# Kernel tuning notes

Measured on AMD Instinct MI355X. Metric: run time of the kernel, lower is better.

The kernel has to match this reference:

```python
import jax, jax.numpy as jnp
import numpy as np

C = 1024
H = 16
DH = C // H
T = 2048
B = 2
EPS = 1e-5


def setup_inputs() -> dict:
    key = jax.random.key(0)
    ks = jax.random.split(key, 11)
    s = 1.0 / np.sqrt(C)
    return {
        "x": jax.random.normal(ks[0], (B, C, T), dtype=jnp.float32),
        "Wq": jax.random.normal(ks[1], (C, C), dtype=jnp.float32) * s,
        "bq": jax.random.normal(ks[2], (C,), dtype=jnp.float32) * 0.01,
        "Wk": jax.random.normal(ks[3], (C, C), dtype=jnp.float32) * s,
        "bk": jax.random.normal(ks[4], (C,), dtype=jnp.float32) * 0.01,
        "Wv": jax.random.normal(ks[5], (C, C), dtype=jnp.float32) * s,
        "bv": jax.random.normal(ks[6], (C,), dtype=jnp.float32) * 0.01,
        "Wo": jax.random.normal(ks[7], (C, C), dtype=jnp.float32) * s,
        "bo": jax.random.normal(ks[8], (C,), dtype=jnp.float32) * 0.01,
        "gamma": jax.random.normal(ks[9], (C,), dtype=jnp.float32) * 0.1,
        "beta": jax.random.normal(ks[10], (C,), dtype=jnp.float32) * 0.1,
    }


def reference(x, Wq, bq, Wk, bk, Wv, bv, Wo, bo, gamma, beta):
    scale = DH ** (-0.5)
    # conv1x1 projections: [B,C,T] x [C_out,C_in] -> [B,C,T]
    q = jnp.einsum('bct,dc->bdt', x, Wq) + bq[None, :, None]
    k = jnp.einsum('bct,dc->bdt', x, Wk) + bk[None, :, None]
    v = jnp.einsum('bct,dc->bdt', x, Wv) + bv[None, :, None]
    # split heads: [B,C,T] -> [B,H,Dh,T]
    q = q.reshape(B, H, DH, T).transpose(0, 1, 3, 2) * scale  # [B,H,T,Dh]
    k = k.reshape(B, H, DH, T)                                # [B,H,Dh,T]
    v = v.reshape(B, H, DH, T).transpose(0, 1, 3, 2)          # [B,H,T,Dh]
    sim = jnp.einsum('bhtd,bhds->bhts', q, k)                 # [B,H,T,T]
    attn = jax.nn.softmax(sim, axis=-1)
    attn = jnp.nan_to_num(attn, nan=0.0)
    out = jnp.einsum('bhts,bhsd->bhtd', attn, v)              # [B,H,T,Dh]
    out = out.transpose(0, 1, 3, 2).reshape(B, C, T)          # [B,C,T]
    y = jnp.einsum('bct,dc->bdt', out, Wo) + bo[None, :, None]
    # BatchNorm1d (training mode: batch statistics over B and T)
    mean = jnp.mean(y, axis=(0, 2), keepdims=True)
    var = jnp.var(y, axis=(0, 2), keepdims=True)
    y = (y - mean) * jax.lax.rsqrt(var + EPS)
    y = y * gamma[None, :, None] + beta[None, :, None]
    return x + y
```

## Files before the change

### kernel.cpp

```cpp
#include <hip/hip_runtime.h>

#define CC 1024
#define HH 16
#define DHH 64
#define TT 2048
#define BB 2

typedef short s8v __attribute__((ext_vector_type(8)));
typedef unsigned short u16x8 __attribute__((ext_vector_type(8)));
typedef float f32x4 __attribute__((ext_vector_type(4)));
typedef float f32x16 __attribute__((ext_vector_type(16)));

__device__ __forceinline__ unsigned short f2bf(float f) {
    union { float f; unsigned int u; } v; v.f = f;
    unsigned int r = v.u + 0x7FFFu + ((v.u >> 16) & 1u);
    return (unsigned short)(r >> 16);
}

__device__ __forceinline__ float bf2f(unsigned short u) {
    union { unsigned int u; float f; } v; v.u = ((unsigned int)u) << 16; return v.f;
}

__device__ __forceinline__ float fexp2(float x) {
#if __has_builtin(__builtin_amdgcn_exp2f)
    return __builtin_amdgcn_exp2f(x);
#else
    return exp2f(x);
#endif
}

__device__ __forceinline__ void gl_lds16(const unsigned short* g, unsigned short* l) {
    __builtin_amdgcn_global_load_lds(
        (const __attribute__((address_space(1))) unsigned int*)g,
        (__attribute__((address_space(3))) unsigned int*)l, 16, 0, 0);
}

__device__ __forceinline__ s8v lds_ld(const unsigned short* base, int byteoff) {
    return *(const s8v*)((const char*)base + byteoff);
}

__device__ __forceinline__ int xcd_swz(int orig, int nwg) {
    int cpx = nwg >> 3;
    return (orig & 7) * cpx + (orig >> 3);
}

__global__ __launch_bounds__(256)
void prep_kernel(const float* __restrict__ x,
                 const float* __restrict__ Wq, const float* __restrict__ Wk,
                 const float* __restrict__ Wv, const float* __restrict__ Wo,
                 unsigned short* __restrict__ Wb, unsigned short* __restrict__ xT) {
    __shared__ float tile[32][33];
    const int tid = threadIdx.x;
    const int bid = blockIdx.x;
    if (bid < 4096) {
        int i = bid * 256 + tid;
        int which = i >> 18;
        int j = (i & 0x3FFFF) * 4;
        const float* s = (which == 0) ? Wq : (which == 1) ? Wk : (which == 2) ? Wv : Wo;
        float4 v = *(const float4*)(s + j);
        unsigned short* d = Wb + (size_t)which * 1048576 + j;
        ushort4 pk; pk.x = f2bf(v.x); pk.y = f2bf(v.y); pk.z = f2bf(v.z); pk.w = f2bf(v.w);
        *(ushort4*)d = pk;
    } else {
        int tb = bid - 4096;
        int t0 = (tb & 63) * 32, c0 = ((tb >> 6) & 31) * 32;
        int b = tb >> 11;
        int tx = tid & 31, ty = tid >> 5;
        const float* xb = x + (size_t)b * CC * TT;
        #pragma unroll
        for (int i = 0; i < 32; i += 8)
            tile[ty + i][tx] = xb[(size_t)(c0 + ty + i) * TT + t0 + tx];
        __syncthreads();
        unsigned short* xTb = xT + (size_t)b * TT * CC;
        #pragma unroll
        for (int i = 0; i < 32; i += 8)
            xTb[(size_t)(t0 + ty + i) * CC + c0 + tx] = f2bf(tile[tx][ty + i]);
    }
}

template<int NFRAG>
__device__ __forceinline__ void gemm_core_k1024(
    const unsigned short* __restrict__ A, const unsigned short* __restrict__ Bt,
    unsigned short* As, unsigned short* Bs,
    int m0, int n0, int tid, f32x4 (&acc)[4][NFRAG]) {
    const int w = tid >> 6, l = tid & 63;
    const int ln = l & 15, hi = l >> 4;
    const int wm = (w >> 1) * 64, wn = (w & 1) * (NFRAG * 16);
    const int BSZ = NFRAG * 1024;
    int offA[4], offB[NFRAG];
    #pragma unroll
    for (int i = 0; i < 4; ++i) {
        int ra = wm + 16 * i + ln;
        offA[i] = ra * 64 + ((hi ^ ((ra >> 1) & 3)) * 16);
    }
    #pragma unroll
    for (int j = 0; j < NFRAG; ++j) {
        int rb = wn + 16 * j + ln;
        offB[j] = rb * 64 + ((hi ^ ((rb >> 1) & 3)) * 16);
    }
    const unsigned short* ap[2];
    const unsigned short* bp[NFRAG / 2];
    #pragma unroll
    for (int j = 0; j < 2; ++j) {
        int p = j * 256 + tid;
        int r = p >> 2, g = (p & 3) ^ ((r >> 1) & 3);
        ap[j] = A + (size_t)(m0 + r) * CC + 8 * g;
    }
    #pragma unroll
    for (int j = 0; j < NFRAG / 2; ++j) {
        int p = j * 256 + tid;
        int r = p >> 2, g = (p & 3) ^ ((r >> 1) & 3);
        bp[j] = Bt + (size_t)(n0 + r) * CC + 8 * g;
    }
    auto stage = [&](int buf) {
        #pragma unroll
        for (int j = 0; j < 2; ++j) {
            gl_lds16(ap[j], As + buf * 4096 + (j * 256 + w * 64) * 8);
            ap[j] += 32;
        }
        #pragma unroll
        for (int j = 0; j < NFRAG / 2; ++j) {
            gl_lds16(bp[j], Bs + buf * BSZ + (j * 256 + w * 64) * 8);
            bp[j] += 32;
        }
    };
    stage(0); stage(1); stage(2);
    if constexpr (NFRAG == 4) asm volatile("s_waitcnt vmcnt(8)" ::: "memory");
    else                      asm volatile("s_waitcnt vmcnt(6)" ::: "memory");
    __builtin_amdgcn_sched_barrier(0);
    __builtin_amdgcn_s_barrier();
    __builtin_amdgcn_sched_barrier(0);
    int buf = 0;
    for (int kk = 0; kk < 32; ++kk) {
        const unsigned short* Ab = As + buf * 4096;
        const unsigned short* Bb = Bs + buf * BSZ;
        s8v a[4], bb[NFRAG];
        #pragma unroll
        for (int i = 0; i < 4; ++i) a[i] = lds_ld(Ab, offA[i]);
        #pragma unroll
        for (int j = 0; j < NFRAG; ++j) bb[j] = lds_ld(Bb, offB[j]);
        __builtin_amdgcn_s_setprio(1);
        #pragma unroll
        for (int i = 0; i < 4; ++i)
            #pragma unroll
            for (int jj = 0; jj < NFRAG; ++jj)
                acc[i][jj] = __builtin_amdgcn_mfma_f32_16x16x32_bf16(a[i], bb[jj], acc[i][jj], 0, 0, 0);
        __builtin_amdgcn_s_setprio(0);
        if (kk < 31) {
            if (kk < 29) {
                if constexpr (NFRAG == 4) asm volatile("s_waitcnt vmcnt(4)" ::: "memory");
                else                      asm volatile("s_waitcnt vmcnt(3)" ::: "memory");
            } else {
                asm volatile("s_waitcnt vmcnt(0)" ::: "memory");
            }
            __builtin_amdgcn_sched_barrier(0);
            __builtin_amdgcn_s_barrier();
            __builtin_amdgcn_sched_barrier(0);
            if (kk < 29) stage(buf);
            buf = (buf == 2) ? 0 : buf + 1;
        }
    }
}

__global__ __launch_bounds__(256, 3)
void gemm_qkv(const unsigned short* __restrict__ xT, const unsigned short* __restrict__ Wb,
              unsigned short* __restrict__ qTp, unsigned short* __restrict__ kTp,
              unsigned short* __restrict__ vp,
              const float* __restrict__ bq, const float* __restrict__ bk,
              const float* __restrict__ bv, float qscale) {
    __shared__ unsigned short As[3 * 4096];
    __shared__ unsigned short Bs[3 * 4096];
    const int tid = threadIdx.x;
    const int wgid = xcd_swz(blockIdx.x, 768);
    const int z = wgid >> 7, bx = wgid & 127;
    const int which = z >> 1, b = z & 1;
    const long TC = (long)TT * CC;

    const unsigned short* A; const unsigned short* Bt;
    int m0, n0;
    if (which < 2) {
        A = xT + (size_t)b * TC;
        Bt = Wb + (size_t)which * 1048576;
        n0 = (bx & 7) * 128; m0 = (bx >> 3) * 128;
    } else {
        A = Wb + 2097152;
        Bt = xT + (size_t)b * TC;
        n0 = (bx & 15) * 128; m0 = (bx >> 4) * 128;
    }

    f32x4 acc[4][4] = {};
    gemm_core_k1024<4>(A, Bt, As, Bs, m0, n0, tid, acc);

    const int w = tid >> 6, l = tid & 63;
    const int ln = l & 15, hi = l >> 4;
    const int wm = (w >> 1) * 64, wn = (w & 1) * 64;

    if (which < 2) {
        unsigned short* Out = (which == 0 ? qTp : kTp) + (size_t)b * TC;
        const float* bias = (which == 0) ? bq : bk;
        float scale = (which == 0) ? qscale : 1.0f;
        #pragma unroll
        for (int i = 0; i < 4; ++i)
            #pragma unroll
            for (int jj = 0; jj < 4; ++jj) {
                int col = n0 + wn + 16 * jj + ln;
                float bvv = bias[col];
                #pragma unroll
                for (int r = 0; r < 4; ++r) {
                    int row = m0 + wm + 16 * i + hi * 4 + r;
                    Out[(size_t)row * CC + col] = f2bf((acc[i][jj][r] + bvv) * scale);
                }
            }
    } else {
        unsigned short* Out = vp + (size_t)b * TC;
        #pragma unroll
        for (int i = 0; i < 4; ++i)
            #pragma unroll
            for (int r = 0; r < 4; ++r) {
                int row = m0 + wm + 16 * i + hi * 4 + r;
                float bvv = bv[row];
                #pragma unroll
                for (int jj = 0; jj < 4; ++jj) {
                    int col = n0 + wn + 16 * jj + ln;
                    Out[(size_t)row * TT + col] = f2bf(acc[i][jj][r] + bvv);
                }
            }
    }
}

__global__ __launch_bounds__(256, 2)
void gemm_y(const unsigned short* __restrict__ Wo, const unsigned short* __restrict__ outT,
            unsigned short* __restrict__ yb, const float* __restrict__ bo) {
    __shared__ unsigned short As[3 * 4096];
    __shared__ unsigned short Bs[3 * 2048];
    const int tid = threadIdx.x;
    const int wgid = xcd_swz(blockIdx.x, 512);
    const int b = wgid >> 8, bx = wgid & 255;
    const int n0 = (bx & 31) * 64, m0 = (bx >> 5) * 128;
    const long TC = (long)TT * CC;

    f32x4 acc[4][2] = {};
    gemm_core_k1024<2>(Wo, outT + (size_t)b * TC, As, Bs, m0, n0, tid, acc);

    const int w = tid >> 6, l = tid & 63;
    const int ln = l & 15, hi = l >> 4;
    const int wm = (w >> 1) * 64, wn = (w & 1) * 32;
    unsigned short* Out = yb + (size_t)b * TC;
    #pragma unroll
    for (int i = 0; i < 4; ++i)
        #pragma unroll
        for (int r = 0; r < 4; ++r) {
            int row = m0 + wm + 16 * i + hi * 4 + r;
            float bvv = bo[row];
            #pragma unroll
            for (int jj = 0; jj < 2; ++jj) {
                int col = n0 + wn + 16 * jj + ln;
                Out[(size_t)row * TT + col] = f2bf(acc[i][jj][r] + bvv);
            }
        }
}

__global__ __launch_bounds__(512, 2)
void attn_kernel(const unsigned short* __restrict__ qT,
                 const unsigned short* __restrict__ kT,
                 const unsigned short* __restrict__ vv,
                 unsigned short* __restrict__ oT) {
    __shared__ unsigned short Ks[2][128 * 64];
    __shared__ unsigned short Vs[2][64 * 128];

    const int tid = threadIdx.x;
    const int w = tid >> 6, l = tid & 63;
    const int l31 = l & 31, h5 = l >> 5, l7 = l & 7;
    const int wgid = xcd_swz(blockIdx.x, 256);
    const int qt0 = (wgid & 7) * 256;
    const int bh = wgid >> 3;
    const int b = bh >> 4, h = bh & 15;
    const size_t bTT = (size_t)b * TT;

    const unsigned short* kp[2];
    const unsigned short* vp2[2];
    #pragma unroll
    for (int j = 0; j < 2; ++j) {
        int c = j * 512 + tid;
        int rk = c >> 3, gk = (c & 7) ^ (rk & 7);
        kp[j] = kT + (bTT + rk) * CC + h * DHH + 8 * gk;
        int rv = c >> 4, gv = (c & 15) ^ (rv & 7);
        vp2[j] = vv + ((size_t)b * CC + h * DHH + rv) * TT + 8 * gv;
    }
    auto stage = [&](int buf) {
        #pragma unroll
        for (int j = 0; j < 2; ++j)
            gl_lds16(kp[j], &Ks[buf][(j * 512 + w * 64) * 8]);
        #pragma unroll
        for (int j = 0; j < 2; ++j)
            gl_lds16(vp2[j], &Vs[buf][(j * 512 + w * 64) * 8]);
        #pragma unroll
        for (int j = 0; j < 2; ++j) { kp[j] += 128 * CC; vp2[j] += 128; }
    };

    stage(0);
    stage(1);

    s8v qf[4];
    {
        const unsigned short* qbase = qT + (bTT + qt0 + w * 32 + l31) * CC + h * DHH + h5 * 8;
        #pragma unroll
        for (int kk = 0; kk < 4; ++kk)
            qf[kk] = *(const s8v*)(qbase + kk * 16);
    }

    int choff[8];
    #pragma unroll
    for (int i = 0; i < 8; ++i) choff[i] = ((2 * i + h5) ^ l7) * 16;
    int rkb[4], rvb[2];
    #pragma unroll
    for (int cb = 0; cb < 4; ++cb) rkb[cb] = (32 * cb + l31) * 128;
    #pragma unroll
    for (int db = 0; db < 2; ++db) rvb[db] = (32 * db + l31) * 256;

    const f32x16 fzero = {};
    f32x16 sf[4];
    f32x16 of0a = {}, of0b = {}, of1a = {}, of1b = {};
    float li = 0.f;

    asm volatile("s_waitcnt vmcnt(4)" ::: "memory");
    __builtin_amdgcn_sched_barrier(0);
    __builtin_amdgcn_s_barrier();
    __builtin_amdgcn_sched_barrier(0);

    auto qk = [&](int buf) {
        const unsigned short* Kb = &Ks[buf][0];
        __builtin_amdgcn_s_setprio(1);
        #pragma unroll
        for (int cb = 0; cb < 4; ++cb) {
            s8v kf0 = lds_ld(Kb, rkb[cb] + choff[0]);
            f32x16 t = __builtin_amdgcn_mfma_f32_32x32x16_bf16(kf0, qf[0], fzero, 0, 0, 0);
            #pragma unroll
            for (int kk = 1; kk < 4; ++kk) {
                s8v kf = lds_ld(Kb, rkb[cb] + choff[kk]);
                t = __builtin_amdgcn_mfma_f32_32x32x16_bf16(kf, qf[kk], t, 0, 0, 0);
            }
            sf[cb] = t;
        }
        __builtin_amdgcn_s_setprio(0);
    };

    qk(0);

    for (int ti = 0; ti < 16; ++ti) {
        const unsigned short* Vb = &Vs[ti & 1][0];
        float ps = 0.f;
        #pragma unroll
        for (int cb = 0; cb < 4; ++cb) {
            unsigned int w8[4][2];
            #pragma unroll
            for (int q3 = 0; q3 < 4; ++q3) {
                float p0 = fexp2(sf[cb][4 * q3 + 0]);
                float p1 = fexp2(sf[cb][4 * q3 + 1]);
                float p2 = fexp2(sf[cb][4 * q3 + 2]);
                float p3 = fexp2(sf[cb][4 * q3 + 3]);
                ps += (p0 + p1) + (p2 + p3);
                asm("v_cvt_pk_bf16_f32 %0, %1, %2" : "=v"(w8[q3][0]) : "v"(p0), "v"(p1));
                asm("v_cvt_pk_bf16_f32 %0, %1, %2" : "=v"(w8[q3][1]) : "v"(p2), "v"(p3));
            }
            {
                unsigned int X0 = w8[0][0], Y0 = w8[1][0];
                unsigned int X1 = w8[0][1], Y1 = w8[1][1];
                asm("v_permlane32_swap_b32 %0, %1" : "+v"(X0), "+v"(Y0));
                asm("v_permlane32_swap_b32 %0, %1" : "+v"(X1), "+v"(Y1));
                union { unsigned int u[4]; s8v v; } up;
                up.u[0] = X0; up.u[1] = X1; up.u[2] = Y0; up.u[3] = Y1;
                s8v vb0 = lds_ld(Vb, rvb[0] + choff[2 * cb]);
                s8v vb1 = lds_ld(Vb, rvb[1] + choff[2 * cb]);
                __builtin_amdgcn_s_setprio(1);
                of0a = __builtin_amdgcn_mfma_f32_32x32x16_bf16(up.v, vb0, of0a, 0, 0, 0);
                of1a = __builtin_amdgcn_mfma_f32_32x32x16_bf16(up.v, vb1, of1a, 0, 0, 0);
                __builtin_amdgcn_s_setprio(0);
            }
            {
                unsigned int X0 = w8[2][0], Y0 = w8[3][0];
                unsigned int X1 = w8[2][1], Y1 = w8[3][1];
                asm("v_permlane32_swap_b32 %0, %1" : "+v"(X0), "+v"(Y0));
                asm("v_permlane32_swap_b32 %0, %1" : "+v"(X1), "+v"(Y1));
                union { unsigned int u[4]; s8v v; } up;
                up.u[0] = X0; up.u[1] = X1; up.u[2] = Y0; up.u[3] = Y1;
                s8v vb0 = lds_ld(Vb, rvb[0] + choff[2 * cb + 1]);
                s8v vb1 = lds_ld(Vb, rvb[1] + choff[2 * cb + 1]);
                __builtin_amdgcn_s_setprio(1);
                of0b = __builtin_amdgcn_mfma_f32_32x32x16_bf16(up.v, vb0, of0b, 0, 0, 0);
                of1b = __builtin_amdgcn_mfma_f32_32x32x16_bf16(up.v, vb1, of1b, 0, 0, 0);
                __builtin_amdgcn_s_setprio(0);
            }
        }
        li += ps;

        if (ti < 15) {
            asm volatile("s_waitcnt vmcnt(0)" ::: "memory");
            __builtin_amdgcn_sched_barrier(0);
            __builtin_amdgcn_s_barrier();
            __builtin_amdgcn_sched_barrier(0);
            if (ti < 14) stage(ti & 1);
            qk((ti + 1) & 1);
        }
    }

    f32x16 o0 = of0a + of0b;
    f32x16 o1 = of1a + of1b;
    li += __shfl_xor(li, 32);
    float inv = 1.0f / li;
    #pragma unroll
    for (int q3 = 0; q3 < 4; ++q3)
        #pragma unroll
        for (int s = 0; s < 4; ++s) {
            float iv = __shfl(inv, 8 * q3 + s + 4 * h5);
            int row = qt0 + w * 32 + 8 * q3 + s + 4 * h5;
            size_t base = (bTT + row) * CC + h * DHH + l31;
            oT[base] = f2bf(o0[4 * q3 + s] * iv);
            oT[base + 32] = f2bf(o1[4 * q3 + s] * iv);
        }
}

__global__ __launch_bounds__(256)
void bn_apply(const float* __restrict__ x, const unsigned short* __restrict__ y,
              const float* __restrict__ gamma, const float* __restrict__ beta,
              float* __restrict__ out) {
    __shared__ unsigned short ys[2][TT];
    const int c = blockIdx.x;
    const int tid = threadIdx.x;
    const unsigned short* y0 = y + (size_t)c * TT;
    const unsigned short* y1 = y + (size_t)(CC + c) * TT;

    float s = 0.f, ss = 0.f;
    {
        int t = tid * 8;
        u16x8 a = *(const u16x8*)(y0 + t);
        u16x8 d = *(const u16x8*)(y1 + t);
        *(u16x8*)(&ys[0][t]) = a;
        *(u16x8*)(&ys[1][t]) = d;
        #pragma unroll
        for (int j = 0; j < 8; ++j) {
            float va = bf2f(a[j]), vd = bf2f(d[j]);
            s += va + vd;
            ss += va * va + vd * vd;
        }
    }
    #pragma unroll
    for (int m = 1; m < 64; m <<= 1) { s += __shfl_xor(s, m); ss += __shfl_xor(ss, m); }
    __shared__ float a1[4], a2[4];
    __shared__ float sMean, sRstd;
    int wv = tid >> 6;
    if ((tid & 63) == 0) { a1[wv] = s; a2[wv] = ss; }
    __syncthreads();
    if (tid == 0) {
        float S = a1[0] + a1[1] + a1[2] + a1[3];
        float SS = a2[0] + a2[1] + a2[2] + a2[3];
        const float inv_n = 1.0f / (BB * TT);
        float mu = S * inv_n;
        sMean = mu;
        sRstd = rsqrtf(SS * inv_n - mu * mu + 1e-5f);
    }
    __syncthreads();
    float a = gamma[c] * sRstd;
    float bb = beta[c] - sMean * a;

    const float* x0 = x + (size_t)c * TT;
    const float* x1 = x + (size_t)(CC + c) * TT;
    float* o0 = out + (size_t)c * TT;
    float* o1 = out + (size_t)(CC + c) * TT;
    {
        int t = tid * 8;
        #pragma unroll
        for (int half = 0; half < 2; ++half) {
            const float* xs = half ? x1 : x0;
            float* os = half ? o1 : o0;
            float4 xv0 = *(const float4*)(xs + t);
            float4 xv1 = *(const float4*)(xs + t + 4);
            float4 o;
            o.x = xv0.x + a * bf2f(ys[half][t + 0]) + bb;
            o.y = xv0.y + a * bf2f(ys[half][t + 1]) + bb;
            o.z = xv0.z + a * bf2f(ys[half][t + 2]) + bb;
            o.w = xv0.w + a * bf2f(ys[half][t + 3]) + bb;
            *(float4*)(os + t) = o;
            o.x = xv1.x + a * bf2f(ys[half][t + 4]) + bb;
            o.y = xv1.y + a * bf2f(ys[half][t + 5]) + bb;
            o.z = xv1.z + a * bf2f(ys[half][t + 6]) + bb;
            o.w = xv1.w + a * bf2f(ys[half][t + 7]) + bb;
            *(float4*)(os + t + 4) = o;
        }
    }
}

extern "C" void kernel_launch(void* const* d_in, const int* in_sizes, int n_in,
                              void* d_out, int out_size, void* d_ws, size_t ws_size,
                              hipStream_t stream) {
    const float* x     = (const float*)d_in[0];
    const float* Wq    = (const float*)d_in[1];
    const float* bq    = (const float*)d_in[2];
    const float* Wk    = (const float*)d_in[3];
    const float* bk    = (const float*)d_in[4];
    const float* Wv    = (const float*)d_in[5];
    const float* bv    = (const float*)d_in[6];
    const float* Wo    = (const float*)d_in[7];
    const float* bo    = (const float*)d_in[8];
    const float* gamma = (const float*)d_in[9];
    const float* beta  = (const float*)d_in[10];
    float* out = (float*)d_out;

    char* ws = (char*)d_ws;
    unsigned short* buf0 = (unsigned short*)(ws);
    unsigned short* Wb   = (unsigned short*)(ws + 8388608);
    unsigned short* qTp  = (unsigned short*)(ws + 16777216);
    unsigned short* kTp  = (unsigned short*)(ws + 25165824);
    unsigned short* vp   = (unsigned short*)(ws + 33554432);
    unsigned short* yb   = (unsigned short*)(ws + 16777216);

    prep_kernel<<<dim3(8192), dim3(256), 0, stream>>>(x, Wq, Wk, Wv, Wo, Wb, buf0);

    gemm_qkv<<<dim3(768), dim3(256), 0, stream>>>(
        buf0, Wb, qTp, kTp, vp, bq, bk, bv, 0.125f * 1.4426950408889634f);

    attn_kernel<<<dim3(256), dim3(512), 0, stream>>>(qTp, kTp, vp, buf0);

    gemm_y<<<dim3(512), dim3(256), 0, stream>>>(Wb + 3145728, buf0, yb, bo);

    bn_apply<<<dim3(CC), dim3(256), 0, stream>>>(x, yb, gamma, beta, out);
}
```

Baseline: 115.6 us.

## Interleave next-tile QK MFMAs with current PV MFMAs in attention loop

Restructures the flash-attention inner loop so the exp/convert step for a whole tile runs first. The QK^T MFMAs for the next K tile are then interleaved with the PV MFMAs for the current V tile in one block. This software-pipelines the two matmul phases so LDS loads and MFMA latency overlap. It adds a second barrier before staging and moves staging after the compute, with a separate epilogue for the last tile. Holding 16x2 packed bf16 words plus the next scores raises register pressure, and the initial wait count changes from vmcnt(4) to vmcnt(8).

After: 112.3 us (median of 2 runs). 1.03x faster.

```diff
diff --git a/kernel.cpp b/kernel.cpp
--- a/kernel.cpp
+++ b/kernel.cpp
@@ -323,13 +323,13 @@
     f32x16 of0a = {}, of0b = {}, of1a = {}, of1b = {};
     float li = 0.f;
 
-    asm volatile("s_waitcnt vmcnt(4)" ::: "memory");
+    asm volatile("s_waitcnt vmcnt(8)" ::: "memory");
     __builtin_amdgcn_sched_barrier(0);
     __builtin_amdgcn_s_barrier();
     __builtin_amdgcn_sched_barrier(0);
 
-    auto qk = [&](int buf) {
-        const unsigned short* Kb = &Ks[buf][0];
+    {
+        const unsigned short* Kb = &Ks[0][0];
         __builtin_amdgcn_s_setprio(1);
         #pragma unroll
         for (int cb = 0; cb < 4; ++cb) {
@@ -343,64 +343,99 @@
             sf[cb] = t;
         }
         __builtin_amdgcn_s_setprio(0);
-    };
-
-    qk(0);
+    }
 
     for (int ti = 0; ti < 16; ++ti) {
-        const unsigned short* Vb = &Vs[ti & 1][0];
-        float ps = 0.f;
-        #pragma unroll
-        for (int cb = 0; cb < 4; ++cb) {
-            unsigned int w8[4][2];
-            #pragma unroll
-            for (int q3 = 0; q3 < 4; ++q3) {
-                float p0 = fexp2(sf[cb][4 * q3 + 0]);
-                float p1 = fexp2(sf[cb][4 * q3 + 1]);
-                float p2 = fexp2(sf[cb][4 * q3 + 2]);
-                float p3 = fexp2(sf[cb][4 * q3 + 3]);
-                ps += (p0 + p1) + (p2 + p3);
-                asm("v_cvt_pk_bf16_f32 %0, %1, %2" : "=v"(w8[q3][0]) : "v"(p0), "v"(p1));
-                asm("v_cvt_pk_bf16_f32 %0, %1, %2" : "=v"(w8[q3][1]) : "v"(p2), "v"(p3));
-            }
-            {
-                unsigned int X0 = w8[0][0], Y0 = w8[1][0];
-                unsigned int X1 = w8[0][1], Y1 = w8[1][1];
-                asm("v_permlane32_swap_b32 %0, %1" : "+v"(X0), "+v"(Y0));
-                asm("v_permlane32_swap_b32 %0, %1" : "+v"(X1), "+v"(Y1));
-                union { unsigned int u[4]; s8v v; } up;
-                up.u[0] = X0; up.u[1] = X1; up.u[2] = Y0; up.u[3] = Y1;
-                s8v vb0 = lds_ld(Vb, rvb[0] + choff[2 * cb]);
-                s8v vb1 = lds_ld(Vb, rvb[1] + choff[2 * cb]);
-                __builtin_amdgcn_s_setprio(1);
-                of0a = __builtin_amdgcn_mfma_f32_32x32x16_bf16(up.v, vb0, of0a, 0, 0, 0);
-                of1a = __builtin_amdgcn_mfma_f32_32x32x16_bf16(up.v, vb1, of1a, 0, 0, 0);
-                __builtin_amdgcn_s_setprio(0);
-            }
-            {
-                unsigned int X0 = w8[2][0], Y0 = w8[3][0];
-                unsigned int X1 = w8[2][1], Y1 = w8[3][1];
-                asm("v_permlane32_swap_b32 %0, %1" : "+v"(X0), "+v"(Y0));
-                asm("v_permlane32_swap_b32 %0, %1" : "+v"(X1), "+v"(Y1));
-                union { unsigned int u[4]; s8v v; } up;
-                up.u[0] = X0; up.u[1] = X1; up.u[2] = Y0; up.u[3] = Y1;
-                s8v vb0 = lds_ld(Vb, rvb[0] + choff[2 * cb + 1]);
-                s8v vb1 = lds_ld(Vb, rvb[1] + choff[2 * cb + 1]);
-                __builtin_amdgcn_s_setprio(1);
-                of0b = __builtin_amdgcn_mfma_f32_32x32x16_bf16(up.v, vb0, of0b, 0, 0, 0);
-                of1b = __builtin_amdgcn_mfma_f32_32x32x16_bf16(up.v, vb1, of1b, 0, 0, 0);
-                __builtin_amdgcn_s_setprio(0);
-            }
-        }
-        li += ps;
+        unsigned int pw[16][2];
+        {
+            float ps = 0.f;
+            #pragma unroll
+            for (int cb = 0; cb < 4; ++cb)
+                #pragma unroll
+                for (int q3 = 0; q3 < 4; ++q3) {
+                    float p0 = fexp2(sf[cb][4 * q3 + 0]);
+                    float p1 = fexp2(sf[cb][4 * q3 + 1]);
+                    float p2 = fexp2(sf[cb][4 * q3 + 2]);
+                    float p3 = fexp2(sf[cb][4 * q3 + 3]);
+                    ps += (p0 + p1) + (p2 + p3);
+                    asm("v_cvt_pk_bf16_f32 %0, %1, %2" : "=v"(pw[4 * cb + q3][0]) : "v"(p0), "v"(p1));
+                    asm("v_cvt_pk_bf16_f32 %0, %1, %2" : "=v"(pw[4 * cb + q3][1]) : "v"(p2), "v"(p3));
+                }
+            li += ps;
+        }
 
         if (ti < 15) {
             asm volatile("s_waitcnt vmcnt(0)" ::: "memory");
             __builtin_amdgcn_sched_barrier(0);
             __builtin_amdgcn_s_barrier();
             __builtin_amdgcn_sched_barrier(0);
+
+            const unsigned short* Kb = &Ks[(ti + 1) & 1][0];
+            const unsigned short* Vb = &Vs[ti & 1][0];
+            __builtin_amdgcn_s_setprio(1);
+            #pragma unroll
+            for (int cb = 0; cb < 4; ++cb) {
+                s8v kf0 = lds_ld(Kb, rkb[cb] + choff[0]);
+                s8v kf1 = lds_ld(Kb, rkb[cb] + choff[1]);
+                s8v kf2 = lds_ld(Kb, rkb[cb] + choff[2]);
+                s8v kf3 = lds_ld(Kb, rkb[cb] + choff[3]);
+                f32x16 t = __builtin_amdgcn_mfma_f32_32x32x16_bf16(kf0, qf[0], fzero, 0, 0, 0);
+                t = __builtin_amdgcn_mfma_f32_32x32x16_bf16(kf1, qf[1], t, 0, 0, 0);
+                {
+                    unsigned int X0 = pw[4 * cb + 0][0], Y0 = pw[4 * cb + 1][0];
+                    unsigned int X1 = pw[4 * cb + 0][1], Y1 = pw[4 * cb + 1][1];
+                    asm("v_permlane32_swap_b32 %0, %1" : "+v"(X0), "+v"(Y0));
+                    asm("v_permlane32_swap_b32 %0, %1" : "+v"(X1), "+v"(Y1));
+                    union { unsigned int u[4]; s8v v; } up;
+                    up.u[0] = X0; up.u[1] = X1; up.u[2] = Y0; up.u[3] = Y1;
+                    s8v vb0 = lds_ld(Vb, rvb[0] + choff[2 * cb]);
+                    s8v vb1 = lds_ld(Vb, rvb[1] + choff[2 * cb]);
+                    of0a = __builtin_amdgcn_mfma_f32_32x32x16_bf16(up.v, vb0, of0a, 0, 0, 0);
+                    of1a = __builtin_amdgcn_mfma_f32_32x32x16_bf16(up.v, vb1, of1a, 0, 0, 0);
+                }
+                t = __builtin_amdgcn_mfma_f32_32x32x16_bf16(kf2, qf[2], t, 0, 0, 0);
+                t = __builtin_amdgcn_mfma_f32_32x32x16_bf16(kf3, qf[3], t, 0, 0, 0);
+                {
+                    unsigned int X0 = pw[4 * cb + 2][0], Y0 = pw[4 * cb + 3][0];
+                    unsigned int X1 = pw[4 * cb + 2][1], Y1 = pw[4 * cb + 3][1];
+                    asm("v_permlane32_swap_b32 %0, %1" : "+v"(X0), "+v"(Y0));
+                    asm("v_permlane32_swap_b32 %0, %1" : "+v"(X1), "+v"(Y1));
+                    union { unsigned int u[4]; s8v v; } up;
+                    up.u[0] = X0; up.u[1] = X1; up.u[2] = Y0; up.u[3] = Y1;
+                    s8v vb0 = lds_ld(Vb, rvb[0] + choff[2 * cb + 1]);
+                    s8v vb1 = lds_ld(Vb, rvb[1] + choff[2 * cb + 1]);
+                    of0b = __builtin_amdgcn_mfma_f32_32x32x16_bf16(up.v, vb0, of0b, 0, 0, 0);
+                    of1b = __builtin_amdgcn_mfma_f32_32x32x16_bf16(up.v, vb1, of1b, 0, 0, 0);
+                }
+                sf[cb] = t;
+            }
+            __builtin_amdgcn_s_setprio(0);
+
+            __builtin_amdgcn_s_barrier();
+            __builtin_amdgcn_sched_barrier(0);
             if (ti < 14) stage(ti & 1);
-            qk((ti + 1) & 1);
+        } else {
+            const unsigned short* Vb = &Vs[ti & 1][0];
+            __builtin_amdgcn_s_setprio(1);
+            #pragma unroll
+            for (int ks = 0; ks < 8; ++ks) {
+                unsigned int X0 = pw[2 * ks][0], Y0 = pw[2 * ks + 1][0];
+                unsigned int X1 = pw[2 * ks][1], Y1 = pw[2 * ks + 1][1];
+                asm("v_permlane32_swap_b32 %0, %1" : "+v"(X0), "+v"(Y0));
+                asm("v_permlane32_swap_b32 %0, %1" : "+v"(X1), "+v"(Y1));
+                union { unsigned int u[4]; s8v v; } up;
+                up.u[0] = X0; up.u[1] = X1; up.u[2] = Y0; up.u[3] = Y1;
+                s8v vb0 = lds_ld(Vb, rvb[0] + choff[ks]);
+                s8v vb1 = lds_ld(Vb, rvb[1] + choff[ks]);
+                if (ks & 1) {
+                    of0b = __builtin_amdgcn_mfma_f32_32x32x16_bf16(up.v, vb0, of0b, 0, 0, 0);
+                    of1b = __builtin_amdgcn_mfma_f32_32x32x16_bf16(up.v, vb1, of1b, 0, 0, 0);
+                } else {
+                    of0a = __builtin_amdgcn_mfma_f32_32x32x16_bf16(up.v, vb0, of0a, 0, 0, 0);
+                    of1a = __builtin_amdgcn_mfma_f32_32x32x16_bf16(up.v, vb1, of1a, 0, 0, 0);
+                }
+            }
+            __builtin_amdgcn_s_setprio(0);
         }
     }
 
```
